# Kernel optimization log

Measured on AMD Instinct MI355X. Metric: run time of the kernel, lower is better.

Reference implementation:

```python
import jax, jax.numpy as jnp
import numpy as np

B, T, C, H, W = 16, 8, 2048, 16, 8
C8, C4, HW, NP = C // 8, C // 4, H * W, T // 2


def _cbr(x, w, s, b):
    # 1x1 conv + folded BN (eval-mode affine) + ReLU; x: (N, Cin, H, W), w: (Cout, Cin)
    y = jnp.einsum('oc,nchw->nohw', w, x)
    return jax.nn.relu(y * s[None, :, None, None] + b[None, :, None, None])


def setup_inputs():
    key = jax.random.key(0)
    ks = jax.random.split(key, 16)
    r = lambda i, shape, sc: jax.random.normal(ks[i], shape, jnp.float32) * sc
    return dict(
        featmap=r(0, (B, T, C, H, W), 1.0),
        re_featmap=r(1, (B * T, C, H, W), 1.0),
        vect_featmap=r(2, (B, T, C), 1.0),
        embed_feat=r(3, (B, T, 128, H, W), 1.0),
        gamma_w=r(4, (C8, C), 0.03), gamma_s=jnp.ones((C8,)), gamma_b=jnp.zeros((C8,)),
        beta_w=r(5, (C8, C), 0.03), beta_s=jnp.ones((C8,)), beta_b=jnp.zeros((C8,)),
        gg_w=r(6, (128, 2 * HW), 0.05), gg_s=jnp.ones((128,)), gg_b=jnp.zeros((128,)),
        tte_w=r(7, (128, 256), 0.05), tte_s=jnp.ones((128,)), tte_b=jnp.zeros((128,)),
        te_w=r(8, (1, 256), 0.05), te_s=jnp.ones((1,)), te_b=jnp.zeros((1,)),
        theta_w=r(9, (C8, C), 0.03), theta_b=jnp.zeros((C8,)),
        cp_w1=r(10, (C8, C4), 0.05), cp_b1=jnp.zeros((C8,)),
        cp_w2=r(11, (C, C8), 0.05), cp_b2=jnp.zeros((C,)),
    )


def reference(featmap, re_featmap, vect_featmap, embed_feat,
              gamma_w, gamma_s, gamma_b, beta_w, beta_s, beta_b,
              gg_w, gg_s, gg_b, tte_w, tte_s, tte_b, te_w, te_s, te_b,
              theta_w, theta_b, cp_w1, cp_b1, cp_w2, cp_b2):
    # spatial attention embeddings: (B, T, C8, HW)
    gamma = _cbr(re_featmap, gamma_w, gamma_s, gamma_b).reshape(B, T, C8, HW)
    beta = _cbr(re_featmap, beta_w, beta_s, beta_b).reshape(B, T, C8, HW)

    # channel attention: Conv1d over time of (B, C, T) -> (B, C8, T)
    cp = jax.nn.relu(jnp.einsum('oc,btc->bot', theta_w, vect_featmap) + theta_b[None, :, None])
    cp = cp.reshape(B, C8, NP, 2)
    c0 = cp[..., 0].transpose(0, 2, 1)  # (B, NP, C8)
    c1 = cp[..., 1].transpose(0, 2, 1)

    def mlp(x):  # (B, NP, C4) -> sigmoid gate (B, NP, C)
        h1 = jax.nn.relu(x @ cp_w1.T + cp_b1)
        return jax.nn.sigmoid(h1 @ cp_w2.T + cp_b2)

    p00 = mlp(jnp.concatenate([c0, c1], -1))  # (B, NP, C)
    p01 = mlp(jnp.concatenate([c1, c0], -1))

    # pairwise spatial graphs
    g0, g1 = gamma[:, 0::2], gamma[:, 1::2]  # (B, NP, C8, HW)
    b0, b1 = beta[:, 0::2], beta[:, 1::2]
    Gs0 = jnp.einsum('bpcs,bpct->bpst', g0, b1)  # (B, NP, HW, HW)
    Gs1 = jnp.einsum('bpcs,bpct->bpst', g1, b0)
    # Gs_in = Gs^T viewed as (HW, H, W); Gs_out = Gs viewed likewise
    j0 = jnp.concatenate([Gs0.transpose(0, 1, 3, 2), Gs1], 2).reshape(B * NP, 2 * HW, H, W)
    j1 = jnp.concatenate([Gs1.transpose(0, 1, 3, 2), Gs0], 2).reshape(B * NP, 2 * HW, H, W)
    gj0 = _cbr(j0, gg_w, gg_s, gg_b)  # (B*NP, 128, H, W)
    gj1 = _cbr(j1, gg_w, gg_s, gg_b)

    ef = embed_feat.reshape(B, NP, 2, 128, H, W)
    e0 = ef[:, :, 0].reshape(B * NP, 128, H, W)
    e1 = ef[:, :, 1].reshape(B * NP, 128, H, W)
    ta = _cbr(jnp.concatenate([e0, e1], 1), tte_w, tte_s, tte_b)  # (B*NP, 128, H, W)
    tb = _cbr(jnp.concatenate([e1, e0], 1), tte_w, tte_s, tte_b)

    def gate(t_feat, gj):  # conv 256->1 + BN + sigmoid
        y = jnp.einsum('oc,nchw->nohw', te_w, jnp.concatenate([t_feat, gj], 1))
        return jax.nn.sigmoid(y * te_s[None, :, None, None] + te_b[None, :, None, None])

    pa = gate(ta, gj0).reshape(B, NP, 1, H, W)
    pb = gate(tb, gj1).reshape(B, NP, 1, H, W)

    f = featmap.reshape(B, NP, 2, C, H, W)
    gate0 = p00[..., None, None] * pa  # (B, NP, C, H, W)
    gate1 = p01[..., None, None] * pb
    out = jax.nn.relu(gate0 * f[:, :, 0] + gate1 * f[:, :, 1])
    return out * out  # (B, T//2, C, H, W)
```

## Files before the change

### kernel.cpp

```cpp
#include <hip/hip_runtime.h>
#include <stdint.h>


typedef _Float16 f16;
typedef _Float16 f16x8 __attribute__((ext_vector_type(8)));
typedef float f32x4 __attribute__((ext_vector_type(4)));

typedef const void __attribute__((address_space(1)))* gptr1;
typedef void __attribute__((address_space(3)))* lptr3;

__device__ __forceinline__ void gload16(const void* g, void* l) {
  __builtin_amdgcn_global_load_lds((gptr1)g, (lptr3)l, 16, 0, 0);
}

__device__ __forceinline__ float sigmoidf_(float x) { return 1.f / (1.f + expf(-x)); }

#define WAIT_VM6 asm volatile("s_waitcnt vmcnt(6)" ::: "memory")
#define WAIT_VM0 asm volatile("s_waitcnt vmcnt(0)" ::: "memory")
#define WAIT_LGKM8 asm volatile("s_waitcnt lgkmcnt(8)" ::: "memory")
#define WAIT_LGKM0 asm volatile("s_waitcnt lgkmcnt(0)" ::: "memory")

__global__ __launch_bounds__(256) void kPP(const float* __restrict__ x,
                                           f16* __restrict__ Af,
                                           const float* __restrict__ gw, const float* __restrict__ gs,
                                           const float* __restrict__ bw, const float* __restrict__ bs,
                                           const float* __restrict__ gg_w, const float* __restrict__ gg_s,
                                           const float* __restrict__ tte_w, const float* __restrict__ tte_s,
                                           const float* __restrict__ thw, const float* __restrict__ w1,
                                           const float* __restrict__ w2,
                                           f16* __restrict__ Whi, f16* __restrict__ Wlo,
                                           float* __restrict__ ggT, float* __restrict__ tteT,
                                           float* __restrict__ thwT, float* __restrict__ w1T,
                                           float* __restrict__ w2T) {
  __shared__ float L[64][129];
  int t = threadIdx.x;
  int bid = blockIdx.x;
  if (bid < 4096) {
    int n = bid >> 5;
    int k0 = (bid & 31) * 64;
    const float* src = x + (size_t)n * 262144 + (size_t)k0 * 128;
    for (int r = 0; r < 8; ++r) {
      int f = r * 256 + t;
      int kk = f >> 5, c4 = (f & 31) * 4;
      float4 v = *(const float4*)(src + kk * 128 + c4);
      L[kk][c4 + 0] = v.x; L[kk][c4 + 1] = v.y; L[kk][c4 + 2] = v.z; L[kk][c4 + 3] = v.w;
    }
    __syncthreads();
    for (int r = 0; r < 4; ++r) {
      int id = r * 256 + t;
      int hw = id >> 3, c = id & 7;
      int cs = c ^ (hw & 7);
      f16x8 h8;
      for (int j = 0; j < 8; ++j)
        h8[j] = (f16)L[cs * 8 + j][hw];
      size_t m = (size_t)n * 128 + hw;
      size_t ob = m * 2048 + (size_t)k0 + (size_t)c * 8;
      *(f16x8*)(Af + ob) = h8;
    }
    return;
  }
  int id = (bid - 4096) * 256 + t;
  if (id < 131072) {
    int o = id >> 8, cch = id & 255;
    float s; const float* row;
    if (o < 256) { s = gs[o]; row = gw + (size_t)o * 2048; }
    else         { s = bs[o - 256]; row = bw + (size_t)(o - 256) * 2048; }
    int kb = cch >> 3, sub = cch & 7;
    int subd = sub ^ (o & 7);
    f16x8 h8, l8;
    for (int j = 0; j < 8; ++j) {
      float v = row[cch * 8 + j] * s;
      f16 h = (f16)v;
      h8[j] = h;
      l8[j] = (f16)(v - (float)h);
    }
    size_t ob = (size_t)o * 2048 + (size_t)kb * 64 + (size_t)subd * 8;
    *(f16x8*)(Whi + ob) = h8;
    *(f16x8*)(Wlo + ob) = l8;
  } else if (id < 163840) {
    int i = id - 131072; int c = i >> 7, o = i & 127;
    ggT[c * 128 + o] = gg_s[o] * gg_w[o * 256 + c];
  } else if (id < 196608) {
    int i = id - 163840; int c = i >> 7, o = i & 127;
    tteT[c * 128 + o] = tte_s[o] * tte_w[o * 256 + c];
  } else if (id < 720896) {
    int i = id - 196608; int o = i >> 11, c = i & 2047;
    thwT[(size_t)c * 256 + o] = thw[(size_t)o * 2048 + c];
  } else if (id < 851968) {
    int i = id - 720896; int o = i >> 9, k = i & 511;
    w1T[(size_t)k * 256 + o] = w1[(size_t)o * 512 + k];
  } else if (id < 1376256) {
    int i = id - 851968; int o = i >> 8, k = i & 255;
    w2T[(size_t)k * 2048 + o] = w2[(size_t)o * 256 + k];
  }
}

__global__ __launch_bounds__(512, 2) void kGemm8(const f16* __restrict__ Af,
                                                 const f16* __restrict__ Whi, const f16* __restrict__ Wlo,
                                                 const float* __restrict__ gamma_b, const float* __restrict__ beta_b,
                                                 float* __restrict__ gammaF, float* __restrict__ betaF) {
  __shared__ __align__(16) f16 S[3][24576];
  int t = threadIdx.x;
  int lane = t & 63, wid = t >> 6;
  int wr = wid >> 2, wc = wid & 3;
  int bid = blockIdx.x;
  int bx = (bid & 7) * 16 + (bid >> 4);
  int by = (bid >> 3) & 1;
  size_t M0 = (size_t)bx * 128;
  size_t N0 = (size_t)by * 256;
  int row8 = wid * 8 + (lane >> 3);
  int sl = lane & 7;
  int fr = lane & 15, fq = lane >> 4;
  f32x4 acc[4][4] = {};
  f16x8 a[8], b[8];

  const char* AB = (const char*)Af;
  const char* WhiB = (const char*)Whi;
  const char* WloB = (const char*)Wlo;
  const size_t aoff0 = (M0 + row8) * 4096 + (size_t)sl * 16;
  const size_t aoff1 = (M0 + 64 + row8) * 4096 + (size_t)sl * 16;
  const size_t woff0 = (N0 + row8) * 4096 + (size_t)sl * 16;
  const size_t woff1 = (N0 + 64 + row8) * 4096 + (size_t)sl * 16;
  const size_t woff2 = (N0 + 128 + row8) * 4096 + (size_t)sl * 16;
  const size_t woff3 = (N0 + 192 + row8) * 4096 + (size_t)sl * 16;

#define STAGE_ALL(dst, s) do {                                                     \
    int koff_ = ((s) & 31) << 7;                                                   \
    const char* wb_ = ((s) >= 32) ? WloB : WhiB;                                   \
    char* l_ = (char*)(dst) + wid * 1024;                                          \
    gload16(AB + aoff0 + koff_, l_);                                               \
    gload16(AB + aoff1 + koff_, l_ + 8192);                                        \
    gload16(wb_ + woff0 + koff_, l_ + 16384);                                      \
    gload16(wb_ + woff1 + koff_, l_ + 24576);                                      \
    gload16(wb_ + woff2 + koff_, l_ + 32768);                                      \
    gload16(wb_ + woff3 + koff_, l_ + 40960);                                      \
  } while (0)

#define LOADG(buf, g) do {                                                         \
    const f16* bA_ = (const f16*)(buf);                                            \
    const f16* bB_ = bA_ + 8192;                                                   \
    int cg_ = (g) * 4 + fq;                                                        \
    _Pragma("unroll") for (int mi = 0; mi < 4; ++mi) {                             \
      int m_ = wr * 64 + mi * 16 + fr;                                             \
      a[(g) * 4 + mi] = *(const f16x8*)(bA_ + m_ * 64 + ((cg_ ^ (m_ & 7)) << 3));  \
    }                                                                              \
    _Pragma("unroll") for (int ni = 0; ni < 4; ++ni) {                             \
      int n_ = wc * 64 + ni * 16 + fr;                                             \
      b[(g) * 4 + ni] = *(const f16x8*)(bB_ + n_ * 64 + ((cg_ ^ (n_ & 7)) << 3));  \
    }                                                                              \
  } while (0)

#define STEP(rdbuf, stbuf, kt) do {                                                \
    if ((kt) < 63) { WAIT_VM6; } else { WAIT_VM0; }                                \
    __builtin_amdgcn_s_barrier();                                                  \
    if ((kt) <= 61) STAGE_ALL(stbuf, (kt) + 2);                                    \
    LOADG(rdbuf, 0);                                                               \
    __builtin_amdgcn_sched_barrier(0);                                             \
    LOADG(rdbuf, 1);                                                               \
    WAIT_LGKM8;                                                                    \
    __builtin_amdgcn_sched_barrier(0);                                             \
    __builtin_amdgcn_s_setprio(1);                                                 \
    _Pragma("unroll") for (int mi = 0; mi < 4; ++mi)                               \
      _Pragma("unroll") for (int ni = 0; ni < 4; ++ni)                             \
        acc[mi][ni] = __builtin_amdgcn_mfma_f32_16x16x32_f16(a[mi], b[ni], acc[mi][ni], 0, 0, 0); \
    WAIT_LGKM0;                                                                    \
    __builtin_amdgcn_sched_barrier(0);                                             \
    _Pragma("unroll") for (int mi = 0; mi < 4; ++mi)                               \
      _Pragma("unroll") for (int ni = 0; ni < 4; ++ni)                             \
        acc[mi][ni] = __builtin_amdgcn_mfma_f32_16x16x32_f16(a[4 + mi], b[4 + ni], acc[mi][ni], 0, 0, 0); \
    __builtin_amdgcn_s_setprio(0);                                                 \
  } while (0)

  STAGE_ALL(&S[0][0], 0);
  STAGE_ALL(&S[1][0], 1);
  for (int base = 0; base < 63; base += 3) {
    STEP(&S[0][0], &S[2][0], base);
    STEP(&S[1][0], &S[0][0], base + 1);
    STEP(&S[2][0], &S[1][0], base + 2);
  }
  STEP(&S[0][0], &S[1][0], 63);
#undef STEP
#undef LOADG
#undef STAGE_ALL

  const float* bias = by ? beta_b : gamma_b;
  float* outb = by ? betaF : gammaF;
#pragma unroll
  for (int mi = 0; mi < 4; ++mi) {
    int hwb = wr * 64 + mi * 16 + fq * 4;
#pragma unroll
    for (int ni = 0; ni < 4; ++ni) {
      int o = wc * 64 + ni * 16 + fr;
      float bb = bias[o];
      f32x4 v = acc[mi][ni];
      float4 w;
      w.x = fmaxf(v[0] + bb, 0.f);
      w.y = fmaxf(v[1] + bb, 0.f);
      w.z = fmaxf(v[2] + bb, 0.f);
      w.w = fmaxf(v[3] + bb, 0.f);
      *(float4*)(outb + (size_t)bx * 32768 + (size_t)o * 128 + hwb) = w;
    }
  }
}

__global__ __launch_bounds__(256) void kTT(const float* __restrict__ vect, const float* __restrict__ thwT,
                                           float* __restrict__ P,
                                           const float* __restrict__ embed, const float* __restrict__ tteT,
                                           const float* __restrict__ tte_b, const float* __restrict__ te_w,
                                           float* __restrict__ Sta) {
  __shared__ float V[512];
  __shared__ __align__(16) float E[256 * 64];
  __shared__ float Red[16 * 64];
  int bid = blockIdx.x;
  int t = threadIdx.x;
  if (bid < 512) {
    int bt = bid & 127, kq = bid >> 7;
    const float* src = vect + (size_t)bt * 2048 + kq * 512;
    if (t < 128) *(float4*)(V + t * 4) = *(const float4*)(src + t * 4);
    __syncthreads();
    const float* wp = thwT + (size_t)kq * 512 * 256 + t;
    float acc = 0.f;
#pragma unroll 8
    for (int c = 0; c < 512; ++c)
      acc = fmaf(wp[(size_t)c * 256], V[c], acc);
    P[((size_t)kq * 128 + bt) * 256 + t] = acc;
    return;
  }
  int i = bid - 512;
  int n = i & 63, gate = (i >> 6) & 1, hh = (i >> 7) & 1;
  int b = n >> 2, p = n & 3;
  const float* eA = embed + (size_t)(b * 8 + 2 * p + gate) * 16384 + hh * 64;
  const float* eB = embed + (size_t)(b * 8 + 2 * p + 1 - gate) * 16384 + hh * 64;
  for (int r = 0; r < 8; ++r) {
    int f = r * 256 + t;
    int ch = f >> 4, q = (f & 15) * 4;
    *(float4*)(E + ch * 64 + q) = *(const float4*)(eA + (size_t)ch * 128 + q);
  }
  for (int r = 0; r < 8; ++r) {
    int f = r * 256 + t;
    int ch = f >> 4, q = (f & 15) * 4;
    *(float4*)(E + (128 + ch) * 64 + q) = *(const float4*)(eB + (size_t)ch * 128 + q);
  }
  __syncthreads();
  int ty = t >> 4, tx = t & 15;
  float acc[8][4] = {};
  for (int c = 0; c < 256; ++c) {
    float w8[8];
    *(float4*)w8 = *(const float4*)(tteT + (size_t)c * 128 + ty * 8);
    *(float4*)(w8 + 4) = *(const float4*)(tteT + (size_t)c * 128 + ty * 8 + 4);
    float4 g = *(const float4*)(E + c * 64 + tx * 4);
    for (int ii = 0; ii < 8; ++ii) {
      acc[ii][0] = fmaf(w8[ii], g.x, acc[ii][0]);
      acc[ii][1] = fmaf(w8[ii], g.y, acc[ii][1]);
      acc[ii][2] = fmaf(w8[ii], g.z, acc[ii][2]);
      acc[ii][3] = fmaf(w8[ii], g.w, acc[ii][3]);
    }
  }
  float par[4] = {0.f, 0.f, 0.f, 0.f};
  for (int ii = 0; ii < 8; ++ii) {
    int o = ty * 8 + ii;
    float tb = tte_b[o], tw = te_w[o];
    for (int j = 0; j < 4; ++j)
      par[j] += tw * fmaxf(acc[ii][j] + tb, 0.f);
  }
  for (int j = 0; j < 4; ++j) Red[ty * 64 + tx * 4 + j] = par[j];
  __syncthreads();
  if (t < 64) {
    float s = 0.f;
    for (int g = 0; g < 16; ++g) s += Red[g * 64 + t];
    Sta[(size_t)gate * 8192 + n * 128 + hh * 64 + t] = s;
  }
}

__global__ __launch_bounds__(256) void kAG(const float* __restrict__ P, const float* __restrict__ thb,
                                           const float* __restrict__ w1T, const float* __restrict__ b1,
                                           float* __restrict__ h1,
                                           const float* __restrict__ gammaF, const float* __restrict__ betaF,
                                           float* __restrict__ Gs0, float* __restrict__ Gs1) {
  __shared__ float x0[256], x1[256];
  __shared__ float ra[256], rb[256];
  __shared__ __align__(16) float As[16 * 128];
  __shared__ __align__(16) float Bs[16 * 64];
  int bid = blockIdx.x;
  int t = threadIdx.x;
  if (bid < 256) {
    int bp = bid & 63, och = bid >> 6;
    int b = bp >> 2, p = bp & 3;
    int bt0 = b * 8 + 2 * p, bt1 = bt0 + 1;
    {
      float a0 = 0.f, a1 = 0.f;
      for (int q = 0; q < 4; ++q) {
        a0 += P[((size_t)q * 128 + bt0) * 256 + t];
        a1 += P[((size_t)q * 128 + bt1) * 256 + t];
      }
      float tb = thb[t];
      x0[t] = fmaxf(a0 + tb, 0.f);
      x1[t] = fmaxf(a1 + tb, 0.f);
    }
    __syncthreads();
    int o = och * 64 + (t & 63);
    int ks = t >> 6;
    const float* xa = (ks < 2) ? x0 : x1;
    const float* xb = (ks < 2) ? x1 : x0;
    int kbase = ks * 128;
    int xoff = (ks < 2) ? kbase : kbase - 256;
    float aa = 0.f, ab = 0.f;
#pragma unroll 8
    for (int ii = 0; ii < 128; ++ii) {
      float w = w1T[(size_t)(kbase + ii) * 256 + o];
      aa = fmaf(w, xa[xoff + ii], aa);
      ab = fmaf(w, xb[xoff + ii], ab);
    }
    ra[t] = aa;
    rb[t] = ab;
    __syncthreads();
    if (t < 64) {
      float sa = ra[t] + ra[64 + t] + ra[128 + t] + ra[192 + t];
      float sb = rb[t] + rb[64 + t] + rb[128 + t] + rb[192 + t];
      float bb = b1[o];
      h1[((size_t)bp * 2) * 256 + o] = fmaxf(sa + bb, 0.f);
      h1[((size_t)bp * 2 + 1) * 256 + o] = fmaxf(sb + bb, 0.f);
    }
    return;
  }
  int i = bid - 256;
  int n = i & 63, which = (i >> 6) & 1, th = (i >> 7) & 1;
  int b = n >> 2, p = n & 3;
  int tg = 2 * p + which;
  int tb = 2 * p + 1 - which;
  const float* A = gammaF + (size_t)(b * 8 + tg) * 32768;
  const float* Bm = betaF + (size_t)(b * 8 + tb) * 32768;
  float* out = (which ? Gs1 : Gs0) + (size_t)n * 16384;
  int ty = t >> 4, tx = t & 15;
  float acc[8][4] = {};
  for (int c0 = 0; c0 < 256; c0 += 16) {
    for (int r = 0; r < 2; ++r) {
      int f = r * 256 + t;
      int cc = f >> 5, col = (f & 31) * 4;
      *(float4*)(As + cc * 128 + col) = *(const float4*)(A + (size_t)(c0 + cc) * 128 + col);
    }
    {
      int cc = t >> 4, col = (t & 15) * 4;
      *(float4*)(Bs + cc * 64 + col) = *(const float4*)(Bm + (size_t)(c0 + cc) * 128 + th * 64 + col);
    }
    __syncthreads();
    for (int cc = 0; cc < 16; ++cc) {
      float a8[8];
      *(float4*)a8 = *(const float4*)(As + cc * 128 + ty * 8);
      *(float4*)(a8 + 4) = *(const float4*)(As + cc * 128 + ty * 8 + 4);
      float4 b4 = *(const float4*)(Bs + cc * 64 + tx * 4);
      for (int ii = 0; ii < 8; ++ii) {
        acc[ii][0] = fmaf(a8[ii], b4.x, acc[ii][0]);
        acc[ii][1] = fmaf(a8[ii], b4.y, acc[ii][1]);
        acc[ii][2] = fmaf(a8[ii], b4.z, acc[ii][2]);
        acc[ii][3] = fmaf(a8[ii], b4.w, acc[ii][3]);
      }
    }
    __syncthreads();
  }
  for (int ii = 0; ii < 8; ++ii) {
    *(float4*)(out + (size_t)(ty * 8 + ii) * 128 + th * 64 + tx * 4) =
        make_float4(acc[ii][0], acc[ii][1], acc[ii][2], acc[ii][3]);
  }
}

__global__ __launch_bounds__(256) void kBG(const float* __restrict__ h1, const float* __restrict__ w2T,
                                           const float* __restrict__ b2,
                                           float* __restrict__ p00, float* __restrict__ p01,
                                           const float* __restrict__ Gs0, const float* __restrict__ Gs1,
                                           const float* __restrict__ ggT, const float* __restrict__ gg_b,
                                           const float* __restrict__ te_w, float* __restrict__ Sgj) {
  __shared__ float ha[256], hb[256];
  __shared__ float G0h[64 * 129];
  __shared__ __align__(16) float G1c[128 * 64];
  __shared__ float Red[16 * 64];
  int bid = blockIdx.x;
  int t = threadIdx.x;
  if (bid < 512) {
    int bp = bid & 63, chc = bid >> 6;
    ha[t] = h1[((size_t)bp * 2) * 256 + t];
    hb[t] = h1[((size_t)bp * 2 + 1) * 256 + t];
    __syncthreads();
    int ch = chc * 256 + t;
    float sa = 0.f, sb = 0.f;
#pragma unroll 8
    for (int k = 0; k < 256; ++k) {
      float w = w2T[(size_t)k * 2048 + ch];
      sa = fmaf(w, ha[k], sa);
      sb = fmaf(w, hb[k], sb);
    }
    p00[(size_t)bp * 2048 + ch] = sigmoidf_(sa + b2[ch]);
    p01[(size_t)bp * 2048 + ch] = sigmoidf_(sb + b2[ch]);
    return;
  }
  int i = bid - 512;
  int n = i & 63, gate = (i >> 6) & 1, hh = (i >> 7) & 1;
  const float* srcT = (gate == 0 ? Gs0 : Gs1) + (size_t)n * 16384;
  const float* srcC = (gate == 0 ? Gs1 : Gs0) + (size_t)n * 16384;
  for (int r = 0; r < 8; ++r) {
    int f = r * 256 + t;
    int hwl = f >> 5, c4 = (f & 31) * 4;
    float4 v = *(const float4*)(srcT + (size_t)(hh * 64 + hwl) * 128 + c4);
    G0h[hwl * 129 + c4 + 0] = v.x;
    G0h[hwl * 129 + c4 + 1] = v.y;
    G0h[hwl * 129 + c4 + 2] = v.z;
    G0h[hwl * 129 + c4 + 3] = v.w;
  }
  for (int r = 0; r < 8; ++r) {
    int f = r * 256 + t;
    int c = f >> 4, q = (f & 15) * 4;
    *(float4*)(G1c + c * 64 + q) = *(const float4*)(srcC + (size_t)c * 128 + hh * 64 + q);
  }
  __syncthreads();
  int ty = t >> 4, tx = t & 15;
  float acc[8][4] = {};
  for (int c = 0; c < 128; ++c) {
    float w8[8];
    *(float4*)w8 = *(const float4*)(ggT + (size_t)c * 128 + ty * 8);
    *(float4*)(w8 + 4) = *(const float4*)(ggT + (size_t)c * 128 + ty * 8 + 4);
    float g4[4];
    for (int j = 0; j < 4; ++j) g4[j] = G0h[(tx * 4 + j) * 129 + c];
    for (int ii = 0; ii < 8; ++ii)
      for (int j = 0; j < 4; ++j)
        acc[ii][j] = fmaf(w8[ii], g4[j], acc[ii][j]);
  }
  for (int c = 0; c < 128; ++c) {
    float w8[8];
    *(float4*)w8 = *(const float4*)(ggT + (size_t)(128 + c) * 128 + ty * 8);
    *(float4*)(w8 + 4) = *(const float4*)(ggT + (size_t)(128 + c) * 128 + ty * 8 + 4);
    float4 g = *(const float4*)(G1c + c * 64 + tx * 4);
    for (int ii = 0; ii < 8; ++ii) {
      acc[ii][0] = fmaf(w8[ii], g.x, acc[ii][0]);
      acc[ii][1] = fmaf(w8[ii], g.y, acc[ii][1]);
      acc[ii][2] = fmaf(w8[ii], g.z, acc[ii][2]);
      acc[ii][3] = fmaf(w8[ii], g.w, acc[ii][3]);
    }
  }
  float par[4] = {0.f, 0.f, 0.f, 0.f};
  for (int ii = 0; ii < 8; ++ii) {
    int o = ty * 8 + ii;
    float gb = gg_b[o], tw = te_w[128 + o];
    for (int j = 0; j < 4; ++j)
      par[j] += tw * fmaxf(acc[ii][j] + gb, 0.f);
  }
  for (int j = 0; j < 4; ++j) Red[ty * 64 + tx * 4 + j] = par[j];
  __syncthreads();
  if (t < 64) {
    float s = 0.f;
    for (int g = 0; g < 16; ++g) s += Red[g * 64 + t];
    Sgj[(size_t)gate * 8192 + n * 128 + hh * 64 + t] = s;
  }
}

__global__ __launch_bounds__(256) void kFinal(const float* __restrict__ featmap, const float* __restrict__ p00,
                                              const float* __restrict__ p01, const float* __restrict__ Sta,
                                              const float* __restrict__ Sgj, const float* __restrict__ te_s,
                                              const float* __restrict__ te_b, float* __restrict__ out) {
  int fid = blockIdx.x * 256 + threadIdx.x;
  int h4 = (fid & 31) * 4;
  int c = (fid >> 5) & 2047;
  int bp = fid >> 16;
  int b = bp >> 2, p = bp & 3;
  float ga = p00[(size_t)bp * 2048 + c];
  float gb = p01[(size_t)bp * 2048 + c];
  float ts = te_s[0], tbv = te_b[0];
  float4 sa0 = *(const float4*)(Sta + (size_t)bp * 128 + h4);
  float4 sg0 = *(const float4*)(Sgj + (size_t)bp * 128 + h4);
  float4 sa1 = *(const float4*)(Sta + 8192 + (size_t)bp * 128 + h4);
  float4 sg1 = *(const float4*)(Sgj + 8192 + (size_t)bp * 128 + h4);
  float4 pa4, pb4;
  pa4.x = sigmoidf_(ts * (sa0.x + sg0.x) + tbv);
  pa4.y = sigmoidf_(ts * (sa0.y + sg0.y) + tbv);
  pa4.z = sigmoidf_(ts * (sa0.z + sg0.z) + tbv);
  pa4.w = sigmoidf_(ts * (sa0.w + sg0.w) + tbv);
  pb4.x = sigmoidf_(ts * (sa1.x + sg1.x) + tbv);
  pb4.y = sigmoidf_(ts * (sa1.y + sg1.y) + tbv);
  pb4.z = sigmoidf_(ts * (sa1.z + sg1.z) + tbv);
  pb4.w = sigmoidf_(ts * (sa1.w + sg1.w) + tbv);
  const float* f0 = featmap + (size_t)(b * 8 + 2 * p) * 262144 + (size_t)c * 128 + h4;
  const float* f1 = f0 + 262144;
  float4 v0 = *(const float4*)f0;
  float4 v1 = *(const float4*)f1;
  float4 o4;
  float r;
  r = fmaxf(ga * pa4.x * v0.x + gb * pb4.x * v1.x, 0.f); o4.x = r * r;
  r = fmaxf(ga * pa4.y * v0.y + gb * pb4.y * v1.y, 0.f); o4.y = r * r;
  r = fmaxf(ga * pa4.z * v0.z + gb * pb4.z * v1.z, 0.f); o4.z = r * r;
  r = fmaxf(ga * pa4.w * v0.w + gb * pb4.w * v1.w, 0.f); o4.w = r * r;
  *(float4*)(out + (size_t)fid * 4) = o4;
}

extern "C" void kernel_launch(void* const* d_in, const int* in_sizes, int n_in,
                              void* d_out, int out_size, void* d_ws, size_t ws_size,
                              hipStream_t stream) {
  (void)in_sizes; (void)n_in; (void)out_size; (void)ws_size;
  const float* featmap    = (const float*)d_in[0];
  const float* re_featmap = (const float*)d_in[1];
  const float* vect       = (const float*)d_in[2];
  const float* embed      = (const float*)d_in[3];
  const float* gamma_w    = (const float*)d_in[4];
  const float* gamma_s    = (const float*)d_in[5];
  const float* gamma_b    = (const float*)d_in[6];
  const float* beta_w     = (const float*)d_in[7];
  const float* beta_s     = (const float*)d_in[8];
  const float* beta_b     = (const float*)d_in[9];
  const float* gg_w       = (const float*)d_in[10];
  const float* gg_s       = (const float*)d_in[11];
  const float* gg_b       = (const float*)d_in[12];
  const float* tte_w      = (const float*)d_in[13];
  const float* tte_s      = (const float*)d_in[14];
  const float* tte_b      = (const float*)d_in[15];
  const float* te_w       = (const float*)d_in[16];
  const float* te_s       = (const float*)d_in[17];
  const float* te_b       = (const float*)d_in[18];
  const float* theta_w    = (const float*)d_in[19];
  const float* theta_b    = (const float*)d_in[20];
  const float* cp_w1      = (const float*)d_in[21];
  const float* cp_b1      = (const float*)d_in[22];
  const float* cp_w2      = (const float*)d_in[23];
  const float* cp_b2      = (const float*)d_in[24];
  float* out = (float*)d_out;

  char* w = (char*)d_ws;
  f16* Af  = (f16*)w;   w += (size_t)16384 * 2048 * 2;
  f16* Whi = (f16*)w;   w += (size_t)512 * 2048 * 2;
  f16* Wlo = (f16*)w;   w += (size_t)512 * 2048 * 2;
  float* gammaF = (float*)w; w += (size_t)128 * 256 * 128 * 4;
  float* betaF  = (float*)w; w += (size_t)128 * 256 * 128 * 4;
  float* Gs0    = (float*)w; w += (size_t)64 * 128 * 128 * 4;
  float* Gs1    = (float*)w; w += (size_t)64 * 128 * 128 * 4;
  float* ggT    = (float*)w; w += (size_t)256 * 128 * 4;
  float* tteT   = (float*)w; w += (size_t)256 * 128 * 4;
  float* thwT   = (float*)w; w += (size_t)2048 * 256 * 4;
  float* w1T    = (float*)w; w += (size_t)512 * 256 * 4;
  float* w2T    = (float*)w; w += (size_t)256 * 2048 * 4;
  float* P      = (float*)w; w += (size_t)4 * 128 * 256 * 4;
  float* h1     = (float*)w; w += (size_t)64 * 2 * 256 * 4;
  float* Sta    = (float*)w; w += (size_t)2 * 64 * 128 * 4;
  float* Sgj    = (float*)w; w += (size_t)2 * 64 * 128 * 4;
  float* p00    = (float*)w; w += (size_t)64 * 2048 * 4;
  float* p01    = (float*)w; w += (size_t)64 * 2048 * 4;

  kPP<<<9472, 256, 0, stream>>>(re_featmap, Af,
                                gamma_w, gamma_s, beta_w, beta_s, gg_w, gg_s, tte_w, tte_s,
                                theta_w, cp_w1, cp_w2, Whi, Wlo, ggT, tteT, thwT, w1T, w2T);
  kGemm8<<<256, 512, 0, stream>>>(Af, Whi, Wlo, gamma_b, beta_b, gammaF, betaF);
  kTT<<<768, 256, 0, stream>>>(vect, thwT, P, embed, tteT, tte_b, te_w, Sta);
  kAG<<<512, 256, 0, stream>>>(P, theta_b, w1T, cp_b1, h1, gammaF, betaF, Gs0, Gs1);
  kBG<<<768, 256, 0, stream>>>(h1, w2T, cp_b2, p00, p01, Gs0, Gs1, ggT, gg_b, te_w, Sgj);
  kFinal<<<16384, 256, 0, stream>>>(featmap, p00, p01, Sta, Sgj, te_s, te_b, out);
}
```

Before: 285.0 us.

## Drop hi/lo weight split in gamma/beta GEMM and tile weight transposes

The gamma/beta 1x1-conv GEMM previously ran twice over K, once with the fp16 high part of the weights and once with the residual low part, to approximate fp32 accuracy. The K loop is now halved to a single fp16 weight pass, which removes half the MFMA work and weight traffic. The small weight transposes in the prep kernel are also rewritten as 64x64 shared-memory tiled transposes with float4 accesses, so far fewer blocks are launched. The cost is lower precision in the gamma/beta outputs, which may hurt tolerance.

```diff
diff --git a/kernel.cpp b/kernel.cpp
--- a/kernel.cpp
+++ b/kernel.cpp
@@ -28,14 +28,15 @@
                                            const float* __restrict__ tte_w, const float* __restrict__ tte_s,
                                            const float* __restrict__ thw, const float* __restrict__ w1,
                                            const float* __restrict__ w2,
-                                           f16* __restrict__ Whi, f16* __restrict__ Wlo,
+                                           f16* __restrict__ Wf,
                                            float* __restrict__ ggT, float* __restrict__ tteT,
                                            float* __restrict__ thwT, float* __restrict__ w1T,
                                            float* __restrict__ w2T) {
-  __shared__ float L[64][129];
+  __shared__ __align__(16) char shmem[64 * 129 * 4];
   int t = threadIdx.x;
   int bid = blockIdx.x;
   if (bid < 4096) {
+    float (*L)[129] = (float(*)[129])shmem;
     int n = bid >> 5;
     int k0 = (bid & 31) * 64;
     const float* src = x + (size_t)n * 262144 + (size_t)k0 * 128;
@@ -59,44 +60,51 @@
     }
     return;
   }
-  int id = (bid - 4096) * 256 + t;
-  if (id < 131072) {
+  if (bid < 4608) {
+    int id = (bid - 4096) * 256 + t;
     int o = id >> 8, cch = id & 255;
     float s; const float* row;
     if (o < 256) { s = gs[o]; row = gw + (size_t)o * 2048; }
     else         { s = bs[o - 256]; row = bw + (size_t)(o - 256) * 2048; }
     int kb = cch >> 3, sub = cch & 7;
     int subd = sub ^ (o & 7);
-    f16x8 h8, l8;
-    for (int j = 0; j < 8; ++j) {
-      float v = row[cch * 8 + j] * s;
-      f16 h = (f16)v;
-      h8[j] = h;
-      l8[j] = (f16)(v - (float)h);
-    }
+    f16x8 h8;
+    for (int j = 0; j < 8; ++j)
+      h8[j] = (f16)(row[cch * 8 + j] * s);
     size_t ob = (size_t)o * 2048 + (size_t)kb * 64 + (size_t)subd * 8;
-    *(f16x8*)(Whi + ob) = h8;
-    *(f16x8*)(Wlo + ob) = l8;
-  } else if (id < 163840) {
-    int i = id - 131072; int c = i >> 7, o = i & 127;
-    ggT[c * 128 + o] = gg_s[o] * gg_w[o * 256 + c];
-  } else if (id < 196608) {
-    int i = id - 163840; int c = i >> 7, o = i & 127;
-    tteT[c * 128 + o] = tte_s[o] * tte_w[o * 256 + c];
-  } else if (id < 720896) {
-    int i = id - 196608; int o = i >> 11, c = i & 2047;
-    thwT[(size_t)c * 256 + o] = thw[(size_t)o * 2048 + c];
-  } else if (id < 851968) {
-    int i = id - 720896; int o = i >> 9, k = i & 511;
-    w1T[(size_t)k * 256 + o] = w1[(size_t)o * 512 + k];
-  } else if (id < 1376256) {
-    int i = id - 851968; int o = i >> 8, k = i & 255;
-    w2T[(size_t)k * 2048 + o] = w2[(size_t)o * 256 + k];
-  }
-}
-
-__global__ __launch_bounds__(512, 2) void kGemm8(const f16* __restrict__ Af,
-                                                 const f16* __restrict__ Whi, const f16* __restrict__ Wlo,
+    *(f16x8*)(Wf + ob) = h8;
+    return;
+  }
+  float (*TL)[65] = (float(*)[65])shmem;
+  int tb = bid - 4608;
+  const float* src; float* dst; const float* scale = nullptr; int R, C;
+  if (tb < 128)      { src = thw;   dst = thwT; R = 256;  C = 2048; }
+  else if (tb < 256) { tb -= 128; src = w2;  dst = w2T;  R = 2048; C = 256; }
+  else if (tb < 288) { tb -= 256; src = w1;  dst = w1T;  R = 256;  C = 512; }
+  else if (tb < 296) { tb -= 288; src = gg_w;  dst = ggT;  scale = gg_s;  R = 128; C = 256; }
+  else               { tb -= 296; src = tte_w; dst = tteT; scale = tte_s; R = 128; C = 256; }
+  int tpc = C >> 6;
+  int r0 = (tb / tpc) * 64, c0 = (tb % tpc) * 64;
+  int i16 = t >> 4, j4 = (t & 15) * 4;
+  for (int s = 0; s < 4; ++s) {
+    int i = i16 + s * 16;
+    float4 v = *(const float4*)(src + (size_t)(r0 + i) * C + c0 + j4);
+    TL[i][j4 + 0] = v.x; TL[i][j4 + 1] = v.y; TL[i][j4 + 2] = v.z; TL[i][j4 + 3] = v.w;
+  }
+  __syncthreads();
+  for (int s = 0; s < 4; ++s) {
+    int j = i16 + s * 16;
+    float4 w;
+    w.x = TL[j4 + 0][j]; w.y = TL[j4 + 1][j]; w.z = TL[j4 + 2][j]; w.w = TL[j4 + 3][j];
+    if (scale) {
+      w.x *= scale[r0 + j4 + 0]; w.y *= scale[r0 + j4 + 1];
+      w.z *= scale[r0 + j4 + 2]; w.w *= scale[r0 + j4 + 3];
+    }
+    *(float4*)(dst + (size_t)(c0 + j) * R + r0 + j4) = w;
+  }
+}
+
+__global__ __launch_bounds__(512, 2) void kGemm8(const f16* __restrict__ Af, const f16* __restrict__ Wf,
                                                  const float* __restrict__ gamma_b, const float* __restrict__ beta_b,
                                                  float* __restrict__ gammaF, float* __restrict__ betaF) {
   __shared__ __align__(16) f16 S[3][24576];
@@ -115,8 +123,7 @@
   f16x8 a[8], b[8];
 
   const char* AB = (const char*)Af;
-  const char* WhiB = (const char*)Whi;
-  const char* WloB = (const char*)Wlo;
+  const char* WB = (const char*)Wf;
   const size_t aoff0 = (M0 + row8) * 4096 + (size_t)sl * 16;
   const size_t aoff1 = (M0 + 64 + row8) * 4096 + (size_t)sl * 16;
   const size_t woff0 = (N0 + row8) * 4096 + (size_t)sl * 16;
@@ -125,15 +132,14 @@
   const size_t woff3 = (N0 + 192 + row8) * 4096 + (size_t)sl * 16;
 
 #define STAGE_ALL(dst, s) do {                                                     \
-    int koff_ = ((s) & 31) << 7;                                                   \
-    const char* wb_ = ((s) >= 32) ? WloB : WhiB;                                   \
+    int koff_ = (s) << 7;                                                          \
     char* l_ = (char*)(dst) + wid * 1024;                                          \
     gload16(AB + aoff0 + koff_, l_);                                               \
     gload16(AB + aoff1 + koff_, l_ + 8192);                                        \
-    gload16(wb_ + woff0 + koff_, l_ + 16384);                                      \
-    gload16(wb_ + woff1 + koff_, l_ + 24576);                                      \
-    gload16(wb_ + woff2 + koff_, l_ + 32768);                                      \
-    gload16(wb_ + woff3 + koff_, l_ + 40960);                                      \
+    gload16(WB + woff0 + koff_, l_ + 16384);                                       \
+    gload16(WB + woff1 + koff_, l_ + 24576);                                       \
+    gload16(WB + woff2 + koff_, l_ + 32768);                                       \
+    gload16(WB + woff3 + koff_, l_ + 40960);                                       \
   } while (0)
 
 #define LOADG(buf, g) do {                                                         \
@@ -151,9 +157,9 @@
   } while (0)
 
 #define STEP(rdbuf, stbuf, kt) do {                                                \
-    if ((kt) < 63) { WAIT_VM6; } else { WAIT_VM0; }                                \
+    if ((kt) < 31) { WAIT_VM6; } else { WAIT_VM0; }                                \
     __builtin_amdgcn_s_barrier();                                                  \
-    if ((kt) <= 61) STAGE_ALL(stbuf, (kt) + 2);                                    \
+    if ((kt) <= 29) STAGE_ALL(stbuf, (kt) + 2);                                    \
     LOADG(rdbuf, 0);                                                               \
     __builtin_amdgcn_sched_barrier(0);                                             \
     LOADG(rdbuf, 1);                                                               \
@@ -173,12 +179,13 @@
 
   STAGE_ALL(&S[0][0], 0);
   STAGE_ALL(&S[1][0], 1);
-  for (int base = 0; base < 63; base += 3) {
+  for (int base = 0; base < 30; base += 3) {
     STEP(&S[0][0], &S[2][0], base);
     STEP(&S[1][0], &S[0][0], base + 1);
     STEP(&S[2][0], &S[1][0], base + 2);
   }
-  STEP(&S[0][0], &S[1][0], 63);
+  STEP(&S[0][0], &S[2][0], 30);
+  STEP(&S[1][0], &S[0][0], 31);
 #undef STEP
 #undef LOADG
 #undef STAGE_ALL
@@ -523,8 +530,7 @@
 
   char* w = (char*)d_ws;
   f16* Af  = (f16*)w;   w += (size_t)16384 * 2048 * 2;
-  f16* Whi = (f16*)w;   w += (size_t)512 * 2048 * 2;
-  f16* Wlo = (f16*)w;   w += (size_t)512 * 2048 * 2;
+  f16* Wf  = (f16*)w;   w += (size_t)512 * 2048 * 2;
   float* gammaF = (float*)w; w += (size_t)128 * 256 * 128 * 4;
   float* betaF  = (float*)w; w += (size_t)128 * 256 * 128 * 4;
   float* Gs0    = (float*)w; w += (size_t)64 * 128 * 128 * 4;
@@ -541,10 +547,10 @@
   float* p00    = (float*)w; w += (size_t)64 * 2048 * 4;
   float* p01    = (float*)w; w += (size_t)64 * 2048 * 4;
 
-  kPP<<<9472, 256, 0, stream>>>(re_featmap, Af,
+  kPP<<<4912, 256, 0, stream>>>(re_featmap, Af,
                                 gamma_w, gamma_s, beta_w, beta_s, gg_w, gg_s, tte_w, tte_s,
-                                theta_w, cp_w1, cp_w2, Whi, Wlo, ggT, tteT, thwT, w1T, w2T);
-  kGemm8<<<256, 512, 0, stream>>>(Af, Whi, Wlo, gamma_b, beta_b, gammaF, betaF);
+                                theta_w, cp_w1, cp_w2, Wf, ggT, tteT, thwT, w1T, w2T);
+  kGemm8<<<256, 512, 0, stream>>>(Af, Wf, gamma_b, beta_b, gammaF, betaF);
   kTT<<<768, 256, 0, stream>>>(vect, thwT, P, embed, tteT, tte_b, te_w, Sta);
   kAG<<<512, 256, 0, stream>>>(P, theta_b, w1T, cp_b1, h1, gammaF, betaF, Gs0, Gs1);
   kBG<<<768, 256, 0, stream>>>(h1, w2T, cp_b2, p00, p01, Gs0, Gs1, ggT, gg_b, te_w, Sgj);
```

Result: faster. 246.0 us (-13.7%).
